# Kernel optimization log

Measured on AMD Instinct MI355X. Metric: run time of the kernel, lower is better.

The kernel has to match this reference:

```python
import jax, jax.numpy as jnp
import numpy as np

DILATIONS = [2 ** i for i in range(9)] * 3  # 27 layers
RD, SD, QD = 32, 512, 256


def conv1d(x, w, b, dilation=1, padding=0):
    # x: [B,C,T], w: [O,I,K], b: [O]
    out = jax.lax.conv_general_dilated(
        x, w, window_strides=(1,), padding=[(padding, padding)],
        rhs_dilation=(dilation,), dimension_numbers=('NCH', 'OIH', 'NCH'))
    return out + b[None, :, None]


def setup_inputs() -> dict:
    key = jax.random.key(0)
    ks = jax.random.split(key, 16)
    T = 131072
    L = len(DILATIONS)
    s = 0.05
    inp = {
        'x': jax.random.normal(ks[0], (1, 1, T), dtype=jnp.float32),
        'Wc': jax.random.normal(ks[1], (RD, 1, 3), dtype=jnp.float32) * s,
        'bc': jnp.zeros((RD,), dtype=jnp.float32),
        'Wt': jax.random.normal(ks[2], (L, RD, RD, 3), dtype=jnp.float32) * s,
        'bt': jnp.zeros((L, RD), dtype=jnp.float32),
        'Ws': jax.random.normal(ks[3], (L, RD, RD, 3), dtype=jnp.float32) * s,
        'bs': jnp.zeros((L, RD), dtype=jnp.float32),
        'Wskip': jax.random.normal(ks[4], (L, SD, RD, 1), dtype=jnp.float32) * s,
        'bskip': jnp.zeros((L, SD), dtype=jnp.float32),
        'Wdense': jax.random.normal(ks[5], (L, RD, RD, 1), dtype=jnp.float32) * s,
        'bdense': jnp.zeros((L, RD), dtype=jnp.float32),
        'Wp1': jax.random.normal(ks[6], (SD, SD, 1), dtype=jnp.float32) * s,
        'bp1': jnp.zeros((SD,), dtype=jnp.float32),
        'Wp2': jax.random.normal(ks[7], (QD, SD, 1), dtype=jnp.float32) * s,
        'bp2': jnp.zeros((QD,), dtype=jnp.float32),
    }
    return inp


def reference(x, Wc, bc, Wt, bt, Ws, bs, Wskip, bskip, Wdense, bdense, Wp1, bp1, Wp2, bp2):
    # causal conv: kernel 3, padding 1 (same length)
    x = conv1d(x, Wc, bc, dilation=1, padding=1)  # [1, RD, T]
    skip = jnp.zeros((1, SD, x.shape[2]), dtype=jnp.float32)
    for i, d in enumerate(DILATIONS):
        xin = x
        g = jnp.tanh(conv1d(x, Wt[i], bt[i], d, d)) * jax.nn.sigmoid(conv1d(x, Ws[i], bs[i], d, d))
        skip = skip + conv1d(g, Wskip[i], bskip[i])
        x = conv1d(g, Wdense[i], bdense[i]) + xin
    # NOTE: the original applies F.relu(x) on the residual path but then
    # overwrites x with the skip-path result, so that relu is dead code.
    out = conv1d(jax.nn.relu(conv1d(skip, Wp1, bp1)), Wp2, bp2)  # [1, QD, T]
    return jax.nn.log_softmax(out, axis=1)
```

## Files before the change

### kernel.cpp

```cpp
#include <hip/hip_runtime.h>

#define T_LEN 131072
#define RD 32
#define SD 512
#define QD 256
#define NL 27
#define KTOT (NL * RD)
#define GPAD 256

typedef __attribute__((ext_vector_type(8))) short short8;
typedef __attribute__((ext_vector_type(4))) float floatx4;

__device__ __forceinline__ unsigned short f2bf(float f) {
    union { float f; unsigned int i; } v; v.f = f;
    unsigned int r = v.i + 0x7fffu + ((v.i >> 16) & 1u);
    return (unsigned short)(r >> 16);
}

__device__ __forceinline__ void gload_lds16(const void* g, void* l) {
    __builtin_amdgcn_global_load_lds(
        (const __attribute__((address_space(1))) unsigned int*)g,
        (__attribute__((address_space(3))) unsigned int*)l, 16, 0, 0);
}

__global__ __launch_bounds__(256)
void k_conv_init(const float* __restrict__ x, const float* __restrict__ Wc,
                 const float* __restrict__ bc,
                 float* __restrict__ xaG, unsigned short* __restrict__ xabG,
                 float* __restrict__ xbG, unsigned short* __restrict__ xbbG)
{
    const int gid = blockIdx.x * 256 + threadIdx.x;

    if (gid < 4 * GPAD * RD) {
        const int region = gid >> 13;
        const int idx = gid & (GPAD * RD - 1);
        float* fg; unsigned short* hg;
        const size_t post = (size_t)(GPAD + T_LEN) * RD;
        switch (region) {
            case 0:  fg = xaG;        hg = xabG;        break;
            case 1:  fg = xaG + post; hg = xabG + post; break;
            case 2:  fg = xbG;        hg = xbbG;        break;
            default: fg = xbG + post; hg = xbbG + post; break;
        }
        fg[idx] = 0.f;
        hg[idx] = 0;
    }

    const int t = gid;
    const float xm = (t > 0) ? x[t - 1] : 0.f;
    const float x0 = x[t];
    const float xp = (t < T_LEN - 1) ? x[t + 1] : 0.f;
    float* row = xaG + (size_t)(GPAD + t) * RD;
    unsigned short* rowb = xabG + (size_t)(GPAD + t) * RD;
#pragma unroll
    for (int o = 0; o < RD; ++o) {
        const float v = bc[o] + Wc[o * 3 + 0] * xm + Wc[o * 3 + 1] * x0 + Wc[o * 3 + 2] * xp;
        row[o] = v;
        rowb[o] = f2bf(v);
    }
}

__global__ __launch_bounds__(256)
void k_wprep(const float* __restrict__ Wt, const float* __restrict__ Ws,
             const float* __restrict__ Wd,
             unsigned short* __restrict__ Wg, unsigned short* __restrict__ Wdb)
{
    const int idx = blockIdx.x * 256 + threadIdx.x;
    const int n1 = NL * 64 * 96;
    const int n2 = NL * RD * RD;
    if (idx < n1) {
        const int l = idx / (64 * 96);
        const int rem = idx % (64 * 96);
        const int m = rem / 96;
        const int k = rem % 96;
        const int j = k / 32;
        const int c = k % 32;
        float v;
        if (m < 32) v = Wt[(((size_t)l * RD + m) * RD + c) * 3 + j];
        else        v = Ws[(((size_t)l * RD + (m - 32)) * RD + c) * 3 + j];
        Wg[idx] = f2bf(v);
    } else if (idx < n1 + n2) {
        const int i2 = idx - n1;
        Wdb[i2] = f2bf(Wd[i2]);
    }
}

__global__ __launch_bounds__(256, 3)
void k_layer_stage(const float* __restrict__ xin,
                   const unsigned short* __restrict__ xinb,
                   float* __restrict__ xout,
                   unsigned short* __restrict__ xoutb,
                   unsigned short* __restrict__ Gt,
                   const unsigned short* __restrict__ Wg,
                   const unsigned short* __restrict__ Wdb,
                   const float* __restrict__ bt, const float* __restrict__ bs,
                   const float* __restrict__ bd, int d, int layer)
{
    __shared__ unsigned short bandsL[3][128 * 32];
    __shared__ float centerL[128 * 32];
    __shared__ unsigned short gtileL[128 * 32];

    const int tid = threadIdx.x;
    const int lane = tid & 63;
    const int w = tid >> 6;
    const int quad = lane >> 4;
    const int l16 = lane & 15;
    const int rbase = w * 32;
    const bool last = (layer == NL - 1);
    const floatx4 vzero = {0.f, 0.f, 0.f, 0.f};

    const int r16c = lane >> 2;
    const int scB = (lane & 3) ^ ((lane >> 3) & 3);
    const int r8c = lane >> 3;
    const int scC = (lane & 7) ^ r8c;
    const long long gbase = (long long)blockIdx.x * 128 + rbase;

#pragma unroll
    for (int j = 0; j < 3; ++j) {
        const long long b0 = gbase + (long long)(j - 1) * d;
#pragma unroll
        for (int i = 0; i < 2; ++i)
            gload_lds16(xinb + (b0 + i * 16 + r16c) * RD + scB * 8,
                        &bandsL[j][(rbase + i * 16) * 32]);
    }
    if (!last) {
#pragma unroll
        for (int i = 0; i < 4; ++i)
            gload_lds16(xin + (gbase + i * 8 + r8c) * RD + scC * 4,
                        &centerL[(rbase + i * 8) * 32]);
        asm volatile("s_waitcnt vmcnt(4)" ::: "memory");
    } else {
        asm volatile("s_waitcnt vmcnt(0)" ::: "memory");
    }

    short8 afr[3][4];
#pragma unroll
    for (int j = 0; j < 3; ++j)
#pragma unroll
        for (int mt = 0; mt < 4; ++mt)
            afr[j][mt] = *reinterpret_cast<const short8*>(
                Wg + (size_t)(mt * 16 + l16) * 96 + j * 32 + quad * 8);

    floatx4 acc[4][2];
#pragma unroll
    for (int mt = 0; mt < 4; ++mt)
#pragma unroll
        for (int nt = 0; nt < 2; ++nt) acc[mt][nt] = vzero;

#pragma unroll
    for (int nt = 0; nt < 2; ++nt) {
        const int rloc = rbase + nt * 16 + l16;
        const int key2 = (rloc >> 1) & 3;
#pragma unroll
        for (int j = 0; j < 3; ++j) {
            const short8 bb = *reinterpret_cast<const short8*>(
                &bandsL[j][rloc * 32 + ((quad ^ key2) * 8)]);
#pragma unroll
            for (int mt = 0; mt < 4; ++mt)
                acc[mt][nt] = __builtin_amdgcn_mfma_f32_16x16x32_bf16(
                    afr[j][mt], bb, acc[mt][nt], 0, 0, 0);
        }
    }

    if (!last) asm volatile("s_waitcnt vmcnt(0)" ::: "memory");

#pragma unroll
    for (int nt = 0; nt < 2; ++nt) {
        const int rloc = rbase + nt * 16 + l16;
        const int key2 = (rloc >> 1) & 3;
        const long long t = (long long)blockIdx.x * 128 + rloc;
#pragma unroll
        for (int pair = 0; pair < 2; ++pair) {
            const floatx4 bt4 = *reinterpret_cast<const floatx4*>(bt + pair * 16 + quad * 4);
            const floatx4 bs4 = *reinterpret_cast<const floatx4*>(bs + pair * 16 + quad * 4);
            ushort4 u;
            unsigned short us[4];
#pragma unroll
            for (int r = 0; r < 4; ++r) {
                const float a1 = acc[pair][nt][r] + bt4[r];
                const float a2 = acc[2 + pair][nt][r] + bs4[r];
                const float th = 1.f - __fdividef(2.f, __expf(2.f * a1) + 1.f);
                const float sg = __fdividef(1.f, 1.f + __expf(-a2));
                us[r] = f2bf(th * sg);
            }
            u.x = us[0]; u.y = us[1]; u.z = us[2]; u.w = us[3];
            const int cbase = pair * 16 + quad * 4;
            if (!last) {
                const int colS = (pair * 2 + (quad >> 1)) ^ key2;
                *reinterpret_cast<ushort4*>(
                    &gtileL[rloc * 32 + colS * 8 + (quad & 1) * 4]) = u;
            }
            *reinterpret_cast<ushort4*>(
                Gt + ((size_t)layer * T_LEN + t) * RD + cbase) = u;
        }
    }

    if (!last) {
        short8 ad[2];
#pragma unroll
        for (int mt = 0; mt < 2; ++mt)
            ad[mt] = *reinterpret_cast<const short8*>(
                Wdb + (size_t)(mt * 16 + l16) * RD + quad * 8);

#pragma unroll
        for (int nt = 0; nt < 2; ++nt) {
            const int rloc = rbase + nt * 16 + l16;
            const int key2 = (rloc >> 1) & 3;
            const long long t = (long long)blockIdx.x * 128 + rloc;
            const short8 bg = *reinterpret_cast<const short8*>(
                &gtileL[rloc * 32 + ((quad ^ key2) * 8)]);
#pragma unroll
            for (int mt = 0; mt < 2; ++mt) {
                const floatx4 a2v = __builtin_amdgcn_mfma_f32_16x16x32_bf16(
                    ad[mt], bg, vzero, 0, 0, 0);
                const int m = mt * 16 + quad * 4;
                const int c16 = (mt * 4 + quad) ^ (rloc & 7);
                const floatx4 xi = *reinterpret_cast<const floatx4*>(
                    &centerL[rloc * 32 + c16 * 4]);
                const floatx4 bd4 = *reinterpret_cast<const floatx4*>(bd + m);
                floatx4 o;
                ushort4 ob;
                o[0] = a2v[0] + bd4[0] + xi[0]; ob.x = f2bf(o[0]);
                o[1] = a2v[1] + bd4[1] + xi[1]; ob.y = f2bf(o[1]);
                o[2] = a2v[2] + bd4[2] + xi[2]; ob.z = f2bf(o[2]);
                o[3] = a2v[3] + bd4[3] + xi[3]; ob.w = f2bf(o[3]);
                *reinterpret_cast<floatx4*>(xout + (size_t)t * RD + m) = o;
                *reinterpret_cast<ushort4*>(xoutb + (size_t)t * RD + m) = ob;
            }
        }
    }
}

__global__ __launch_bounds__(256)
void k_wcomb(const float* __restrict__ Wp1, const float* __restrict__ Wskip,
             unsigned short* __restrict__ Wcomb)
{
    const int idx = blockIdx.x * 256 + threadIdx.x;
    if (idx >= SD * KTOT) return;
    const int m = idx / KTOT;
    const int k = idx % KTOT;
    const int l = k / RD;
    const int c = k % RD;
    const float* wp1r = Wp1 + (size_t)m * SD;
    const float* wsk = Wskip + (size_t)l * SD * RD + c;
    float acc = 0.f;
    for (int j = 0; j < SD; ++j) acc += wp1r[j] * wsk[(size_t)j * RD];
    Wcomb[((size_t)l * SD + m) * RD + c] = f2bf(acc);
}

__global__ __launch_bounds__(512)
void k_hbias(const float* __restrict__ Wp1, const float* __restrict__ bp1,
             const float* __restrict__ bskip, float* __restrict__ hbias)
{
    __shared__ float sb[SD];
    const int tid = threadIdx.x;
    float s = 0.f;
    for (int l = 0; l < NL; ++l) s += bskip[l * SD + tid];
    sb[tid] = s;
    __syncthreads();
    float acc = bp1[tid];
    const float* r = Wp1 + (size_t)tid * SD;
    for (int j = 0; j < SD; ++j) acc += r[j] * sb[j];
    hbias[tid] = acc;
}

__global__ __launch_bounds__(256)
void k_cvt(const float* __restrict__ src, unsigned short* __restrict__ dst, int n)
{
    const int i = blockIdx.x * 256 + threadIdx.x;
    if (i < n) dst[i] = f2bf(src[i]);
}

__global__ __launch_bounds__(256)
void k_gemm1(const unsigned short* __restrict__ A,
             const unsigned short* __restrict__ B,
             const float* __restrict__ hbias,
             unsigned short* __restrict__ ht)
{
    __shared__ unsigned short ldsA[128 * 32];
    __shared__ unsigned short ldsB[128 * 32];
    const int tid = threadIdx.x;
    const int lane = tid & 63;
    const int w = tid >> 6;
    const int wm = w & 1;
    const int wn = w >> 1;
    const int quad = lane >> 4;
    const int l16 = lane & 15;

    const int g = blockIdx.x;
    const int m0 = ((g >> 3) & 3) * 128;
    const int n0 = ((g & 7) + 8 * (g >> 5)) * 128;

    const int r4 = lane >> 2;
    const int c4 = lane & 3;
    const int srcc = c4 ^ ((r4 >> 1) & 3);
    const int swz = (l16 >> 1) & 3;

    floatx4 acc[4][4];
    const floatx4 vzero = {0.f, 0.f, 0.f, 0.f};
#pragma unroll
    for (int mt = 0; mt < 4; ++mt)
#pragma unroll
        for (int nt = 0; nt < 4; ++nt) acc[mt][nt] = vzero;

    const unsigned short* pA = A + (size_t)(m0 + r4) * RD + srcc * 8;
    const unsigned short* pB = B + (size_t)(n0 + r4) * RD + srcc * 8;

    for (int kc = 0; kc < KTOT / 32; ++kc) {
#pragma unroll
        for (int c = 0; c < 2; ++c) {
            const int row = w * 32 + c * 16;
            gload_lds16(pA + ((size_t)kc * SD + row) * RD, &ldsA[(size_t)row * 32]);
            gload_lds16(pB + ((size_t)kc * T_LEN + row) * RD, &ldsB[(size_t)row * 32]);
        }
        __syncthreads();

        short8 afr[4], bfr[4];
#pragma unroll
        for (int mt = 0; mt < 4; ++mt)
            afr[mt] = *reinterpret_cast<const short8*>(
                &ldsA[(wm * 64 + mt * 16 + l16) * 32 + (quad ^ swz) * 8]);
#pragma unroll
        for (int nt = 0; nt < 4; ++nt)
            bfr[nt] = *reinterpret_cast<const short8*>(
                &ldsB[(wn * 64 + nt * 16 + l16) * 32 + (quad ^ swz) * 8]);
#pragma unroll
        for (int mt = 0; mt < 4; ++mt)
#pragma unroll
            for (int nt = 0; nt < 4; ++nt)
                acc[mt][nt] = __builtin_amdgcn_mfma_f32_16x16x32_bf16(afr[mt], bfr[nt], acc[mt][nt], 0, 0, 0);
        __syncthreads();
    }

#pragma unroll
    for (int mt = 0; mt < 4; ++mt) {
        const int m = m0 + wm * 64 + mt * 16 + quad * 4;
        const floatx4 hb = *reinterpret_cast<const floatx4*>(hbias + m);
        const size_t chunkbase = (size_t)(m >> 5) * T_LEN;
        const int mc = m & 31;
#pragma unroll
        for (int nt = 0; nt < 4; ++nt) {
            const int t = n0 + wn * 64 + nt * 16 + l16;
            ushort4 st;
            float v;
            v = acc[mt][nt][0] + hb[0]; st.x = f2bf(v > 0.f ? v : 0.f);
            v = acc[mt][nt][1] + hb[1]; st.y = f2bf(v > 0.f ? v : 0.f);
            v = acc[mt][nt][2] + hb[2]; st.z = f2bf(v > 0.f ? v : 0.f);
            v = acc[mt][nt][3] + hb[3]; st.w = f2bf(v > 0.f ? v : 0.f);
            *reinterpret_cast<ushort4*>(ht + (chunkbase + t) * RD + mc) = st;
        }
    }
}

__global__ __launch_bounds__(256)
void k_gemm2_lsm(const unsigned short* __restrict__ A,
                 const unsigned short* __restrict__ B,
                 const float* __restrict__ bp2,
                 float* __restrict__ out)
{
    __shared__ unsigned short ldsB[64 * 32];
    __shared__ float redmax[4 * 16 * 16];
    __shared__ float redsum[4 * 16 * 16];
    const int tid = threadIdx.x;
    const int lane = tid & 63;
    const int w = tid >> 6;
    const int quad = lane >> 4;
    const int l16 = lane & 15;
    const int m0 = w * 64;
    const int n0 = blockIdx.x * 64;

    const int r4 = lane >> 2;
    const int c4 = lane & 3;
    const int srcc = c4 ^ ((r4 >> 1) & 3);
    const int swz = (l16 >> 1) & 3;

    const unsigned short* ab[4];
#pragma unroll
    for (int mt = 0; mt < 4; ++mt)
        ab[mt] = A + (size_t)(m0 + mt * 16 + l16) * SD + quad * 8;

    const unsigned short* pB = B + (size_t)(n0 + w * 16 + r4) * RD + srcc * 8;

    floatx4 acc[4][4];
    const floatx4 vzero = {0.f, 0.f, 0.f, 0.f};
#pragma unroll
    for (int mt = 0; mt < 4; ++mt)
#pragma unroll
        for (int nt = 0; nt < 4; ++nt) acc[mt][nt] = vzero;

    for (int kc = 0; kc < SD / 32; ++kc) {
        const int k0 = kc * 32;
        gload_lds16(pB + (size_t)kc * T_LEN * RD, &ldsB[(size_t)(w * 16) * 32]);
        short8 afr[4];
#pragma unroll
        for (int mt = 0; mt < 4; ++mt)
            afr[mt] = *reinterpret_cast<const short8*>(ab[mt] + k0);
        __syncthreads();

        short8 bfr[4];
#pragma unroll
        for (int nt = 0; nt < 4; ++nt)
            bfr[nt] = *reinterpret_cast<const short8*>(
                &ldsB[(nt * 16 + l16) * 32 + (quad ^ swz) * 8]);
#pragma unroll
        for (int mt = 0; mt < 4; ++mt)
#pragma unroll
            for (int nt = 0; nt < 4; ++nt)
                acc[mt][nt] = __builtin_amdgcn_mfma_f32_16x16x32_bf16(
                    afr[mt], bfr[nt], acc[mt][nt], 0, 0, 0);
        __syncthreads();
    }

#pragma unroll
    for (int mt = 0; mt < 4; ++mt) {
        const int mb = m0 + mt * 16 + quad * 4;
        const floatx4 bz = *reinterpret_cast<const floatx4*>(bp2 + mb);
#pragma unroll
        for (int nt = 0; nt < 4; ++nt)
#pragma unroll
            for (int j = 0; j < 4; ++j) acc[mt][nt][j] += bz[j];
    }

#pragma unroll
    for (int nt = 0; nt < 4; ++nt) {
        float lm = -1e30f;
#pragma unroll
        for (int mt = 0; mt < 4; ++mt)
#pragma unroll
            for (int j = 0; j < 4; ++j) lm = fmaxf(lm, acc[mt][nt][j]);
        redmax[nt * 256 + l16 * 16 + w * 4 + quad] = lm;
    }
    __syncthreads();

    float lse[4];
#pragma unroll
    for (int nt = 0; nt < 4; ++nt) {
        float gm = -1e30f;
#pragma unroll
        for (int i = 0; i < 16; ++i) gm = fmaxf(gm, redmax[nt * 256 + l16 * 16 + i]);
        float ls = 0.f;
#pragma unroll
        for (int mt = 0; mt < 4; ++mt)
#pragma unroll
            for (int j = 0; j < 4; ++j) ls += __expf(acc[mt][nt][j] - gm);
        redsum[nt * 256 + l16 * 16 + w * 4 + quad] = ls;
        lse[nt] = gm;
    }
    __syncthreads();

#pragma unroll
    for (int nt = 0; nt < 4; ++nt) {
        float tot = 0.f;
#pragma unroll
        for (int i = 0; i < 16; ++i) tot += redsum[nt * 256 + l16 * 16 + i];
        lse[nt] = lse[nt] + __logf(tot);
    }

#pragma unroll
    for (int mt = 0; mt < 4; ++mt) {
        const int mb = m0 + mt * 16 + quad * 4;
#pragma unroll
        for (int nt = 0; nt < 4; ++nt) {
            const int t = n0 + nt * 16 + l16;
#pragma unroll
            for (int j = 0; j < 4; ++j)
                out[(size_t)(mb + j) * T_LEN + t] = acc[mt][nt][j] - lse[nt];
        }
    }
}

extern "C" void kernel_launch(void* const* d_in, const int* in_sizes, int n_in,
                              void* d_out, int out_size, void* d_ws, size_t ws_size,
                              hipStream_t stream)
{
    (void)in_sizes; (void)n_in; (void)out_size; (void)ws_size;
    const float* x     = (const float*)d_in[0];
    const float* Wc    = (const float*)d_in[1];
    const float* bc    = (const float*)d_in[2];
    const float* Wt    = (const float*)d_in[3];
    const float* bt    = (const float*)d_in[4];
    const float* Ws    = (const float*)d_in[5];
    const float* bs    = (const float*)d_in[6];
    const float* Wskip = (const float*)d_in[7];
    const float* bskip = (const float*)d_in[8];
    const float* Wd    = (const float*)d_in[9];
    const float* bd    = (const float*)d_in[10];
    const float* Wp1   = (const float*)d_in[11];
    const float* bp1   = (const float*)d_in[12];
    const float* Wp2   = (const float*)d_in[13];
    const float* bp2   = (const float*)d_in[14];
    float* out = (float*)d_out;

    char* p = (char*)d_ws;
    unsigned short* Gt = (unsigned short*)p;    p += (size_t)T_LEN * KTOT * 2;
    unsigned short* ht = (unsigned short*)p;    p += (size_t)T_LEN * SD * 2;
    unsigned short* Wcomb = (unsigned short*)p; p += (size_t)SD * KTOT * 2;
    unsigned short* Wp2b = (unsigned short*)p;  p += (size_t)QD * SD * 2;
    unsigned short* Wg = (unsigned short*)p;    p += (size_t)NL * 64 * 96 * 2;
    unsigned short* Wdb = (unsigned short*)p;   p += (size_t)NL * RD * RD * 2;
    float* hbias = (float*)p;                   p += (size_t)SD * 4;

    char* q = (char*)ht;
    const size_t grows = (size_t)(T_LEN + 2 * GPAD) * RD;
    float* xaG = (float*)q;                     q += grows * 4;
    float* xbG = (float*)q;                     q += grows * 4;
    unsigned short* xabG = (unsigned short*)q;  q += grows * 2;
    unsigned short* xbbG = (unsigned short*)q;  q += grows * 2;
    float* xa = xaG + (size_t)GPAD * RD;
    float* xb = xbG + (size_t)GPAD * RD;
    unsigned short* xab = xabG + (size_t)GPAD * RD;
    unsigned short* xbb = xbbG + (size_t)GPAD * RD;

    k_wcomb<<<(SD * KTOT + 255) / 256, 256, 0, stream>>>(Wp1, Wskip, Wcomb);
    k_hbias<<<1, 512, 0, stream>>>(Wp1, bp1, bskip, hbias);
    k_cvt<<<(QD * SD + 255) / 256, 256, 0, stream>>>(Wp2, Wp2b, QD * SD);
    {
        const int nprep = NL * 64 * 96 + NL * RD * RD;
        k_wprep<<<(nprep + 255) / 256, 256, 0, stream>>>(Wt, Ws, Wd, Wg, Wdb);
    }
    k_conv_init<<<T_LEN / 256, 256, 0, stream>>>(x, Wc, bc, xaG, xabG, xbG, xbbG);

    static const int dil[NL] = {1, 2, 4, 8, 16, 32, 64, 128, 256,
                                1, 2, 4, 8, 16, 32, 64, 128, 256,
                                1, 2, 4, 8, 16, 32, 64, 128, 256};
    const float* cur = xa;
    const unsigned short* curb = xab;
    float* nxt = xb;
    unsigned short* nxtb = xbb;
    for (int i = 0; i < NL; ++i) {
        k_layer_stage<<<T_LEN / 128, 256, 0, stream>>>(
            cur, curb, nxt, nxtb, Gt,
            Wg + (size_t)i * 64 * 96,
            Wdb + (size_t)i * RD * RD,
            bt + (size_t)i * RD,
            bs + (size_t)i * RD,
            bd + (size_t)i * RD,
            dil[i], i);
        { float* tf = (float*)cur; cur = nxt; nxt = tf; }
        { unsigned short* tb = (unsigned short*)curb; curb = nxtb; nxtb = tb; }
    }

    k_gemm1<<<4 * (T_LEN / 128), 256, 0, stream>>>(Wcomb, Gt, hbias, ht);
    k_gemm2_lsm<<<T_LEN / 64, 256, 0, stream>>>(Wp2b, ht, bp2, out);
}
```

Baseline: 1.016 ms.

## Fuse first five dilation layers per stack into one halo kernel; double-buffer GEMM loads

Adds a kernel that runs layers with dilation 1-16 back to back on a 192-row tile. The tile has a 32-row halo on each side and the residual state stays in LDS, replacing five separate launches and their global round-trips of x. Halo rows are recomputed redundantly, and only the central 128 rows are written out. The two output GEMMs now load two K-chunks per barrier into double LDS buffers, which halves synchronization count at the cost of more LDS.

```diff
diff --git a/kernel.cpp b/kernel.cpp
--- a/kernel.cpp
+++ b/kernel.cpp
@@ -7,6 +7,8 @@
 #define NL 27
 #define KTOT (NL * RD)
 #define GPAD 256
+
+#define G5R 192
 
 typedef __attribute__((ext_vector_type(8))) short short8;
 typedef __attribute__((ext_vector_type(4))) float floatx4;
@@ -85,6 +87,165 @@
     }
 }
 
+__global__ __launch_bounds__(384, 4)
+void k_group5(const float* __restrict__ xin,
+              const unsigned short* __restrict__ xinb,
+              float* __restrict__ xout,
+              unsigned short* __restrict__ xoutb,
+              unsigned short* __restrict__ Gt,
+              const unsigned short* __restrict__ WgAll,
+              const unsigned short* __restrict__ WdbAll,
+              const float* __restrict__ btAll,
+              const float* __restrict__ bsAll,
+              const float* __restrict__ bdAll,
+              int l0)
+{
+    __shared__ float xs[G5R * RD];
+    __shared__ unsigned short xsb[G5R * RD];
+    __shared__ unsigned short gtileL[G5R * RD];
+
+    const int tid = threadIdx.x;
+    const int lane = tid & 63;
+    const int w = tid >> 6;
+    const int quad = lane >> 4;
+    const int l16 = lane & 15;
+    const int rbase = w * 32;
+    const long long t0 = (long long)blockIdx.x * 128;
+    const floatx4 vzero = {0.f, 0.f, 0.f, 0.f};
+    const bool owned = (w >= 1 && w <= 4);
+
+    {
+        const int r8c = lane >> 3;
+        const int scC = (lane & 7) ^ r8c;
+        const int r16c = lane >> 2;
+        const int scB = (lane & 3) ^ ((lane >> 3) & 3);
+        const long long gb = t0 - 32 + rbase;
+#pragma unroll
+        for (int i = 0; i < 4; ++i)
+            gload_lds16(xin + (gb + i * 8 + r8c) * RD + scC * 4,
+                        &xs[(rbase + i * 8) * 32]);
+#pragma unroll
+        for (int i = 0; i < 2; ++i)
+            gload_lds16(xinb + (gb + i * 16 + r16c) * RD + scB * 8,
+                        &xsb[(rbase + i * 16) * 32]);
+    }
+    asm volatile("s_waitcnt vmcnt(0)" ::: "memory");
+    __syncthreads();
+
+#pragma unroll
+    for (int i = 0; i < 5; ++i) {
+        const int d = 1 << i;
+        const int l = l0 + i;
+        const unsigned short* Wg = WgAll + (size_t)l * 64 * 96;
+        const unsigned short* Wdb = WdbAll + (size_t)l * RD * RD;
+        const float* btp = btAll + (size_t)l * RD;
+        const float* bsp = bsAll + (size_t)l * RD;
+        const float* bdp = bdAll + (size_t)l * RD;
+
+        short8 afr[3][4];
+#pragma unroll
+        for (int j = 0; j < 3; ++j)
+#pragma unroll
+            for (int mt = 0; mt < 4; ++mt)
+                afr[j][mt] = *reinterpret_cast<const short8*>(
+                    Wg + (size_t)(mt * 16 + l16) * 96 + j * 32 + quad * 8);
+        short8 ad[2];
+#pragma unroll
+        for (int mt = 0; mt < 2; ++mt)
+            ad[mt] = *reinterpret_cast<const short8*>(
+                Wdb + (size_t)(mt * 16 + l16) * RD + quad * 8);
+
+        floatx4 acc[4][2];
+#pragma unroll
+        for (int mt = 0; mt < 4; ++mt)
+#pragma unroll
+            for (int nt = 0; nt < 2; ++nt) acc[mt][nt] = vzero;
+
+#pragma unroll
+        for (int nt = 0; nt < 2; ++nt) {
+            const int e = rbase + nt * 16 + l16;
+#pragma unroll
+            for (int j = 0; j < 3; ++j) {
+                int et = e + (j - 1) * d;
+                et = et < 0 ? 0 : (et > G5R - 1 ? G5R - 1 : et);
+                const short8 bb = *reinterpret_cast<const short8*>(
+                    &xsb[et * 32 + ((quad ^ ((et >> 1) & 3)) * 8)]);
+#pragma unroll
+                for (int mt = 0; mt < 4; ++mt)
+                    acc[mt][nt] = __builtin_amdgcn_mfma_f32_16x16x32_bf16(
+                        afr[j][mt], bb, acc[mt][nt], 0, 0, 0);
+            }
+        }
+
+#pragma unroll
+        for (int nt = 0; nt < 2; ++nt) {
+            const int e = rbase + nt * 16 + l16;
+            const int key2 = (e >> 1) & 3;
+#pragma unroll
+            for (int pair = 0; pair < 2; ++pair) {
+                const floatx4 bt4 = *reinterpret_cast<const floatx4*>(btp + pair * 16 + quad * 4);
+                const floatx4 bs4 = *reinterpret_cast<const floatx4*>(bsp + pair * 16 + quad * 4);
+                ushort4 u;
+                unsigned short us[4];
+#pragma unroll
+                for (int r = 0; r < 4; ++r) {
+                    const float a1 = acc[pair][nt][r] + bt4[r];
+                    const float a2 = acc[2 + pair][nt][r] + bs4[r];
+                    const float th = 1.f - __fdividef(2.f, __expf(2.f * a1) + 1.f);
+                    const float sg = __fdividef(1.f, 1.f + __expf(-a2));
+                    us[r] = f2bf(th * sg);
+                }
+                u.x = us[0]; u.y = us[1]; u.z = us[2]; u.w = us[3];
+                const int colS = (pair * 2 + (quad >> 1)) ^ key2;
+                *reinterpret_cast<ushort4*>(
+                    &gtileL[e * 32 + colS * 8 + (quad & 1) * 4]) = u;
+                if (owned) {
+                    const long long t = t0 + e - 32;
+                    *reinterpret_cast<ushort4*>(
+                        Gt + ((size_t)l * T_LEN + t) * RD + pair * 16 + quad * 4) = u;
+                }
+            }
+        }
+
+        __syncthreads();
+
+#pragma unroll
+        for (int nt = 0; nt < 2; ++nt) {
+            const int e = rbase + nt * 16 + l16;
+            const int key2 = (e >> 1) & 3;
+            const short8 bg = *reinterpret_cast<const short8*>(
+                &gtileL[e * 32 + ((quad ^ key2) * 8)]);
+#pragma unroll
+            for (int mt = 0; mt < 2; ++mt) {
+                const floatx4 a2v = __builtin_amdgcn_mfma_f32_16x16x32_bf16(
+                    ad[mt], bg, vzero, 0, 0, 0);
+                const int m = mt * 16 + quad * 4;
+                const int slotF = (mt * 4 + quad) ^ (e & 7);
+                const floatx4 xi = *reinterpret_cast<const floatx4*>(
+                    &xs[e * 32 + slotF * 4]);
+                const floatx4 bd4 = *reinterpret_cast<const floatx4*>(bdp + m);
+                floatx4 o;
+                ushort4 ob;
+                o[0] = a2v[0] + bd4[0] + xi[0]; ob.x = f2bf(o[0]);
+                o[1] = a2v[1] + bd4[1] + xi[1]; ob.y = f2bf(o[1]);
+                o[2] = a2v[2] + bd4[2] + xi[2]; ob.z = f2bf(o[2]);
+                o[3] = a2v[3] + bd4[3] + xi[3]; ob.w = f2bf(o[3]);
+                if (i < 4) {
+                    *reinterpret_cast<floatx4*>(&xs[e * 32 + slotF * 4]) = o;
+                    const int slotB = (mt * 2 + (quad >> 1)) ^ key2;
+                    *reinterpret_cast<ushort4*>(
+                        &xsb[e * 32 + slotB * 8 + (quad & 1) * 4]) = ob;
+                } else if (owned) {
+                    const long long t = t0 + e - 32;
+                    *reinterpret_cast<floatx4*>(xout + (size_t)t * RD + m) = o;
+                    *reinterpret_cast<ushort4*>(xoutb + (size_t)t * RD + m) = ob;
+                }
+            }
+        }
+        __syncthreads();
+    }
+}
+
 __global__ __launch_bounds__(256, 3)
 void k_layer_stage(const float* __restrict__ xin,
                    const unsigned short* __restrict__ xinb,
@@ -277,8 +438,8 @@
              const float* __restrict__ hbias,
              unsigned short* __restrict__ ht)
 {
-    __shared__ unsigned short ldsA[128 * 32];
-    __shared__ unsigned short ldsB[128 * 32];
+    __shared__ unsigned short ldsA[2][128 * 32];
+    __shared__ unsigned short ldsB[2][128 * 32];
     const int tid = threadIdx.x;
     const int lane = tid & 63;
     const int w = tid >> 6;
@@ -306,30 +467,63 @@
     const unsigned short* pA = A + (size_t)(m0 + r4) * RD + srcc * 8;
     const unsigned short* pB = B + (size_t)(n0 + r4) * RD + srcc * 8;
 
-    for (int kc = 0; kc < KTOT / 32; ++kc) {
+    for (int kc2 = 0; kc2 < 13; ++kc2) {
+#pragma unroll
+        for (int s = 0; s < 2; ++s) {
+            const int kc = kc2 * 2 + s;
+#pragma unroll
+            for (int c = 0; c < 2; ++c) {
+                const int row = w * 32 + c * 16;
+                gload_lds16(pA + ((size_t)kc * SD + row) * RD, &ldsA[s][row * 32]);
+                gload_lds16(pB + ((size_t)kc * T_LEN + row) * RD, &ldsB[s][row * 32]);
+            }
+        }
+        __syncthreads();
+
+#pragma unroll
+        for (int s = 0; s < 2; ++s) {
+            short8 afr[4], bfr[4];
+#pragma unroll
+            for (int mt = 0; mt < 4; ++mt)
+                afr[mt] = *reinterpret_cast<const short8*>(
+                    &ldsA[s][(wm * 64 + mt * 16 + l16) * 32 + (quad ^ swz) * 8]);
+#pragma unroll
+            for (int nt = 0; nt < 4; ++nt)
+                bfr[nt] = *reinterpret_cast<const short8*>(
+                    &ldsB[s][(wn * 64 + nt * 16 + l16) * 32 + (quad ^ swz) * 8]);
+#pragma unroll
+            for (int mt = 0; mt < 4; ++mt)
+#pragma unroll
+                for (int nt = 0; nt < 4; ++nt)
+                    acc[mt][nt] = __builtin_amdgcn_mfma_f32_16x16x32_bf16(
+                        afr[mt], bfr[nt], acc[mt][nt], 0, 0, 0);
+        }
+        __syncthreads();
+    }
+    {
+        const int kc = 26;
 #pragma unroll
         for (int c = 0; c < 2; ++c) {
             const int row = w * 32 + c * 16;
-            gload_lds16(pA + ((size_t)kc * SD + row) * RD, &ldsA[(size_t)row * 32]);
-            gload_lds16(pB + ((size_t)kc * T_LEN + row) * RD, &ldsB[(size_t)row * 32]);
+            gload_lds16(pA + ((size_t)kc * SD + row) * RD, &ldsA[0][row * 32]);
+            gload_lds16(pB + ((size_t)kc * T_LEN + row) * RD, &ldsB[0][row * 32]);
         }
         __syncthreads();
-
         short8 afr[4], bfr[4];
 #pragma unroll
         for (int mt = 0; mt < 4; ++mt)
             afr[mt] = *reinterpret_cast<const short8*>(
-                &ldsA[(wm * 64 + mt * 16 + l16) * 32 + (quad ^ swz) * 8]);
+                &ldsA[0][(wm * 64 + mt * 16 + l16) * 32 + (quad ^ swz) * 8]);
 #pragma unroll
         for (int nt = 0; nt < 4; ++nt)
             bfr[nt] = *reinterpret_cast<const short8*>(
-                &ldsB[(wn * 64 + nt * 16 + l16) * 32 + (quad ^ swz) * 8]);
+                &ldsB[0][(wn * 64 + nt * 16 + l16) * 32 + (quad ^ swz) * 8]);
 #pragma unroll
         for (int mt = 0; mt < 4; ++mt)
 #pragma unroll
             for (int nt = 0; nt < 4; ++nt)
-                acc[mt][nt] = __builtin_amdgcn_mfma_f32_16x16x32_bf16(afr[mt], bfr[nt], acc[mt][nt], 0, 0, 0);
-        __syncthreads();
+                acc[mt][nt] = __builtin_amdgcn_mfma_f32_16x16x32_bf16(
+                    afr[mt], bfr[nt], acc[mt][nt], 0, 0, 0);
     }
 
 #pragma unroll
@@ -358,7 +552,7 @@
                  const float* __restrict__ bp2,
                  float* __restrict__ out)
 {
-    __shared__ unsigned short ldsB[64 * 32];
+    __shared__ unsigned short ldsB[2][64 * 32];
     __shared__ float redmax[4 * 16 * 16];
     __shared__ float redsum[4 * 16 * 16];
     const int tid = threadIdx.x;
@@ -388,26 +582,32 @@
 #pragma unroll
         for (int nt = 0; nt < 4; ++nt) acc[mt][nt] = vzero;
 
-    for (int kc = 0; kc < SD / 32; ++kc) {
-        const int k0 = kc * 32;
-        gload_lds16(pB + (size_t)kc * T_LEN * RD, &ldsB[(size_t)(w * 16) * 32]);
-        short8 afr[4];
-#pragma unroll
-        for (int mt = 0; mt < 4; ++mt)
-            afr[mt] = *reinterpret_cast<const short8*>(ab[mt] + k0);
+    for (int kc2 = 0; kc2 < 8; ++kc2) {
+        short8 afr[2][4];
+#pragma unroll
+        for (int s = 0; s < 2; ++s) {
+            const int kc = kc2 * 2 + s;
+            gload_lds16(pB + (size_t)kc * T_LEN * RD, &ldsB[s][(w * 16) * 32]);
+#pragma unroll
+            for (int mt = 0; mt < 4; ++mt)
+                afr[s][mt] = *reinterpret_cast<const short8*>(ab[mt] + kc * 32);
+        }
         __syncthreads();
 
-        short8 bfr[4];
-#pragma unroll
-        for (int nt = 0; nt < 4; ++nt)
-            bfr[nt] = *reinterpret_cast<const short8*>(
-                &ldsB[(nt * 16 + l16) * 32 + (quad ^ swz) * 8]);
-#pragma unroll
-        for (int mt = 0; mt < 4; ++mt)
+#pragma unroll
+        for (int s = 0; s < 2; ++s) {
+            short8 bfr[4];
 #pragma unroll
             for (int nt = 0; nt < 4; ++nt)
-                acc[mt][nt] = __builtin_amdgcn_mfma_f32_16x16x32_bf16(
-                    afr[mt], bfr[nt], acc[mt][nt], 0, 0, 0);
+                bfr[nt] = *reinterpret_cast<const short8*>(
+                    &ldsB[s][(nt * 16 + l16) * 32 + (quad ^ swz) * 8]);
+#pragma unroll
+            for (int mt = 0; mt < 4; ++mt)
+#pragma unroll
+                for (int nt = 0; nt < 4; ++nt)
+                    acc[mt][nt] = __builtin_amdgcn_mfma_f32_16x16x32_bf16(
+                        afr[s][mt], bfr[nt], acc[mt][nt], 0, 0, 0);
+        }
         __syncthreads();
     }
 
@@ -520,24 +720,29 @@
     }
     k_conv_init<<<T_LEN / 256, 256, 0, stream>>>(x, Wc, bc, xaG, xabG, xbG, xbbG);
 
-    static const int dil[NL] = {1, 2, 4, 8, 16, 32, 64, 128, 256,
-                                1, 2, 4, 8, 16, 32, 64, 128, 256,
-                                1, 2, 4, 8, 16, 32, 64, 128, 256};
     const float* cur = xa;
     const unsigned short* curb = xab;
     float* nxt = xb;
     unsigned short* nxtb = xbb;
-    for (int i = 0; i < NL; ++i) {
-        k_layer_stage<<<T_LEN / 128, 256, 0, stream>>>(
-            cur, curb, nxt, nxtb, Gt,
-            Wg + (size_t)i * 64 * 96,
-            Wdb + (size_t)i * RD * RD,
-            bt + (size_t)i * RD,
-            bs + (size_t)i * RD,
-            bd + (size_t)i * RD,
-            dil[i], i);
+    static const int dsing[4] = {32, 64, 128, 256};
+    for (int s = 0; s < 3; ++s) {
+        k_group5<<<T_LEN / 128, 384, 0, stream>>>(
+            cur, curb, nxt, nxtb, Gt, Wg, Wdb, bt, bs, bd, 9 * s);
         { float* tf = (float*)cur; cur = nxt; nxt = tf; }
         { unsigned short* tb = (unsigned short*)curb; curb = nxtb; nxtb = tb; }
+        for (int j = 0; j < 4; ++j) {
+            const int li = 9 * s + 5 + j;
+            k_layer_stage<<<T_LEN / 128, 256, 0, stream>>>(
+                cur, curb, nxt, nxtb, Gt,
+                Wg + (size_t)li * 64 * 96,
+                Wdb + (size_t)li * RD * RD,
+                bt + (size_t)li * RD,
+                bs + (size_t)li * RD,
+                bd + (size_t)li * RD,
+                dsing[j], li);
+            { float* tf = (float*)cur; cur = nxt; nxt = tf; }
+            { unsigned short* tb = (unsigned short*)curb; curb = nxtb; nxtb = tb; }
+        }
     }
 
     k_gemm1<<<4 * (T_LEN / 128), 256, 0, stream>>>(Wcomb, Gt, hbias, ht);
```

After: 973.7 us. 1.04x faster.
